# Kernel tuning notes

Hardware: AMD Instinct MI355X
Metric: run time of the kernel (lower is better)

The kernel has to match this reference:

```python
import jax, jax.numpy as jnp
import numpy as np


def setup_inputs() -> dict:
    key = jax.random.key(0)
    ks = jax.random.split(key, 8)
    B, C, W, H = 4, 256, 64, 64
    dqk = C // 8
    s_in = 1.0 / np.sqrt(C)
    return {
        "x": jax.random.normal(ks[0], (B, C, W, H), dtype=jnp.float32),
        "Wq": jax.random.normal(ks[1], (dqk, C), dtype=jnp.float32) * s_in,
        "bq": jnp.zeros((dqk,), dtype=jnp.float32),
        "Wk": jax.random.normal(ks[2], (dqk, C), dtype=jnp.float32) * s_in,
        "bk": jnp.zeros((dqk,), dtype=jnp.float32),
        "Wv": jax.random.normal(ks[3], (C, C), dtype=jnp.float32) * s_in,
        "bv": jnp.zeros((C,), dtype=jnp.float32),
        "gamma": jnp.zeros((1,), dtype=jnp.float32),
    }


def reference(x, Wq, bq, Wk, bk, Wv, bv, gamma):
    B, C, W, H = x.shape
    N = W * H
    xf = x.reshape(B, C, N)  # flatten spatial: B x C x N
    # 1x1 convs == per-pixel linear projections over channels
    q = jnp.einsum("bcn,dc->bnd", xf, Wq) + bq            # B x N x dqk
    k = jnp.einsum("bcn,dc->bdn", xf, Wk) + bk[None, :, None]  # B x dqk x N
    v = jnp.einsum("bcn,dc->bdn", xf, Wv) + bv[None, :, None]  # B x C x N
    # unscaled attention, softmax over keys (last dim)
    attn = jax.nn.softmax(jnp.einsum("bnd,bdm->bnm", q, k), axis=-1)  # B x N x N
    # out[b,c,i] = sum_j v[b,c,j] * attn[b,i,j]  (bmm with attn^T)
    out = jnp.einsum("bcj,bij->bci", v, attn).reshape(B, C, W, H)
    return gamma[0] * out + x
```

## Files before the change

### kernel.cpp

```cpp
#include <hip/hip_runtime.h>

#define BB 4
#define CC 256
#define NN 4096

typedef __attribute__((ext_vector_type(8))) short bh8;
typedef __attribute__((ext_vector_type(4))) float f32x4;

#define WPK_OFF  0
#define BALL_OFF 163840
#define QBF_OFF  165888
#define KBF_OFF  (165888 + 1048576)
#define VBF_OFF  (165888 + 2097152)

typedef const __attribute__((address_space(1))) void* gas_t;
typedef __attribute__((address_space(3))) void* las_t;
__device__ inline void gld16(const void* g, void* l) {
    __builtin_amdgcn_global_load_lds((gas_t)g, (las_t)l, 16, 0, 0);
}

__device__ inline int pack2bf(float a, float b) {
    unsigned ua = __builtin_bit_cast(unsigned, a) + 0x8000u;
    unsigned ub = __builtin_bit_cast(unsigned, b) + 0x8000u;
    return (int)__builtin_amdgcn_perm(ub, ua, 0x07060302u);
}
__device__ inline short f2bf1(float a) {
    return (short)((__builtin_bit_cast(unsigned, a) + 0x8000u) >> 16);
}

__global__ __launch_bounds__(256) void prep_w(const float* __restrict__ Wq,
        const float* __restrict__ bq, const float* __restrict__ Wk,
        const float* __restrict__ bk, const float* __restrict__ Wv,
        const float* __restrict__ bv, short* __restrict__ Wpk,
        float* __restrict__ ball) {
    int tid = blockIdx.x * 256 + threadIdx.x;
    if (tid < 10240) {
        int lane = tid & 63;
        int fc = tid >> 6;
        int mt = fc >> 3, ck = fc & 7;
        int m = mt * 16 + (lane & 15);
        int c0 = ck * 32 + (lane >> 4) * 8;
        const float* wrow;
        if (m < 32)      wrow = Wq + m * 256;
        else if (m < 64) wrow = Wk + (m - 32) * 256;
        else             wrow = Wv + (m - 64) * 256;
        int d[4];
        #pragma unroll
        for (int p = 0; p < 4; ++p)
            d[p] = pack2bf(wrow[c0 + 2 * p], wrow[c0 + 2 * p + 1]);
        *(int4*)(Wpk + tid * 8) = make_int4(d[0], d[1], d[2], d[3]);
    }
    if (tid < 320) {
        float b2 = tid < 32 ? bq[tid] : (tid < 64 ? bk[tid - 32] : bv[tid - 64]);
        ball[tid] = b2;
    }
}

__global__ __launch_bounds__(256) void proj(const float* __restrict__ x,
        const short* __restrict__ Wpk, const float* __restrict__ ball,
        short* __restrict__ qbf, short* __restrict__ kbf,
        short* __restrict__ vbf) {
    int t = threadIdx.x;
    int w = t >> 6, lane = t & 63, quad = lane >> 4, c15 = lane & 15;
    int gw = blockIdx.x * 4 + w;
    int tile = gw >> 1, mh = gw & 1;
    int b = tile >> 8, n0 = (tile & 255) * 16;
    const float* xb = x + (size_t)b * CC * NN;

    bh8 af[8];
    #pragma unroll
    for (int ck = 0; ck < 8; ++ck) {
        float v[8];
        #pragma unroll
        for (int e = 0; e < 8; ++e)
            v[e] = xb[(size_t)(ck * 32 + quad * 8 + e) * NN + n0 + c15];
        int d[4];
        #pragma unroll
        for (int p = 0; p < 4; ++p) d[p] = pack2bf(v[2 * p], v[2 * p + 1]);
        af[ck] = __builtin_bit_cast(bh8, make_int4(d[0], d[1], d[2], d[3]));
    }

    #pragma unroll
    for (int mpi = 0; mpi < 5; ++mpi) {
        int mp = mh * 5 + mpi;
        int mtA = mp * 2, mtB = mp * 2 + 1;
        float blA = ball[mtA * 16 + c15], blB = ball[mtB * 16 + c15];
        f32x4 accA = {blA, blA, blA, blA}, accB = {blB, blB, blB, blB};
        #pragma unroll
        for (int ck = 0; ck < 8; ++ck) {
            bh8 wfA = *(const bh8*)(Wpk + ((mtA * 8 + ck) * 64 + lane) * 8);
            bh8 wfB = *(const bh8*)(Wpk + ((mtB * 8 + ck) * 64 + lane) * 8);
            accA = __builtin_amdgcn_mfma_f32_16x16x32_bf16(af[ck], wfA, accA, 0, 0, 0);
            accB = __builtin_amdgcn_mfma_f32_16x16x32_bf16(af[ck], wfB, accB, 0, 0, 0);
        }
        #pragma unroll
        for (int half = 0; half < 2; ++half) {
            int mt = mp * 2 + half;
            f32x4 acc = half ? accB : accA;
            if (mt < 4) {
                short* dst = (mt < 2) ? qbf : kbf;
                int m = (mt & 1) * 16 + c15;
                #pragma unroll
                for (int r = 0; r < 4; ++r)
                    dst[(size_t)(b * NN + n0 + quad * 4 + r) * 32 + m] = f2bf1(acc[r]);
            } else {
                int c = mt * 16 + c15 - 64;
                int2 pk;
                pk.x = pack2bf(acc[0], acc[1]);
                pk.y = pack2bf(acc[2], acc[3]);
                *(int2*)(vbf + (size_t)b * CC * NN + (size_t)c * NN + n0 + quad * 4) = pk;
            }
        }
    }
}

__global__ __launch_bounds__(512, 2) void flash_attn(
        const short* __restrict__ qbf, const short* __restrict__ kbf,
        const short* __restrict__ vbf, const float* __restrict__ x,
        const float* __restrict__ gamma, float* __restrict__ out) {
    __shared__ char lds[82944];

    int bid = blockIdx.x;
    int b = bid & 3, i0 = (bid >> 2) * 64;
    int t = threadIdx.x;
    int w = t >> 6, lane = t & 63, quad = lane >> 4, c15 = lane & 15;
    int mg = w & 3, nh = w >> 2, jsub = w & 3;

    const short* qb = qbf + (size_t)b * NN * 32;
    const short* kb = kbf + (size_t)b * NN * 32;
    const short* vb = vbf + (size_t)b * CC * NN;

    bh8 qf0 = *(const bh8*)(qb + (size_t)(i0 + nh * 32 + c15) * 32 + quad * 8);
    bh8 qf1 = *(const bh8*)(qb + (size_t)(i0 + nh * 32 + 16 + c15) * 32 + quad * 8);

    int vrow = w * 32 + (lane >> 3);
    int glog = (lane & 7) ^ ((lane >> 3) & 7);
    const short* vsg = vb + (size_t)vrow * NN + glog * 8;
    char* vdst = lds + w * 4096;

    const short* kptr = kb + (size_t)(jsub * 16 + c15) * 32 + quad * 8;

    char* Pt = lds + 65536;
    float* lred = (float*)(lds + 81920);

    f32x4 acc[4][2];
    #pragma unroll
    for (int ms = 0; ms < 4; ++ms) {
        acc[ms][0] = (f32x4){0.f, 0.f, 0.f, 0.f};
        acc[ms][1] = (f32x4){0.f, 0.f, 0.f, 0.f};
    }
    float lsum0 = 0.f, lsum1 = 0.f;
    const f32x4 initc = {-12.f, -12.f, -12.f, -12.f};

    #pragma unroll
    for (int r = 0; r < 4; ++r) gld16(vsg + r * 8 * NN, vdst + r * 1024);
    bh8 kf = *(const bh8*)kptr;
    __syncthreads();

    for (int jt = 0; jt < 64; ++jt) {
        int cur = jt & 1;
        f32x4 sa0 = __builtin_amdgcn_mfma_f32_16x16x32_bf16(kf, qf0, initc, 0, 0, 0);
        f32x4 sa1 = __builtin_amdgcn_mfma_f32_16x16x32_bf16(kf, qf1, initc, 0, 0, 0);
        bh8 kfn = *(const bh8*)(kptr + (size_t)((jt + 1) & 63) * 2048);
        float p0[4], p1[4];
        #pragma unroll
        for (int r = 0; r < 4; ++r) {
            p0[r] = __expf(sa0[r]); lsum0 += p0[r];
            p1[r] = __expf(sa1[r]); lsum1 += p1[r];
        }
        char* Ptc = Pt + cur * 8192;
        int g = jsub * 2 + (quad >> 1);
        int pb0 = (nh * 32 + c15) * 128 + ((g ^ (c15 & 7)) * 16) + (quad & 1) * 8;
        *(int2*)(Ptc + pb0) = make_int2(pack2bf(p0[0], p0[1]), pack2bf(p0[2], p0[3]));
        *(int2*)(Ptc + pb0 + 2048) = make_int2(pack2bf(p1[0], p1[1]), pack2bf(p1[2], p1[3]));

        __syncthreads();

        if (jt < 63) {
            const short* vs = vsg + (jt + 1) * 64;
            char* vd = vdst + ((cur ^ 1) << 15);
            #pragma unroll
            for (int r = 0; r < 4; ++r) gld16(vs + r * 8 * NN, vd + r * 1024);
        }

        const char* Vb = lds + cur * 32768;
        #pragma unroll
        for (int kk = 0; kk < 2; ++kk) {
            int gs = ((kk * 4 + quad) ^ (c15 & 7)) * 16;
            bh8 pfa = *(const bh8*)(Ptc + (nh * 32 + c15) * 128 + gs);
            bh8 pfb = *(const bh8*)(Ptc + (nh * 32 + 16 + c15) * 128 + gs);
            #pragma unroll
            for (int ms = 0; ms < 4; ++ms) {
                int c = mg * 64 + ms * 16 + c15;
                bh8 vf = *(const bh8*)(Vb + c * 128 + gs);
                acc[ms][0] = __builtin_amdgcn_mfma_f32_16x16x32_bf16(vf, pfa, acc[ms][0], 0, 0, 0);
                acc[ms][1] = __builtin_amdgcn_mfma_f32_16x16x32_bf16(vf, pfb, acc[ms][1], 0, 0, 0);
            }
        }
        kf = kfn;
    }

    lsum0 += __shfl_xor(lsum0, 16); lsum0 += __shfl_xor(lsum0, 32);
    lsum1 += __shfl_xor(lsum1, 16); lsum1 += __shfl_xor(lsum1, 32);
    __syncthreads();
    if (lane < 16) {
        lred[w * 32 + lane] = lsum0;
        lred[w * 32 + 16 + lane] = lsum1;
    }
    __syncthreads();
    float l0 = lred[(nh * 4 + 0) * 32 + c15] + lred[(nh * 4 + 1) * 32 + c15]
             + lred[(nh * 4 + 2) * 32 + c15] + lred[(nh * 4 + 3) * 32 + c15];
    float l1 = lred[(nh * 4 + 0) * 32 + 16 + c15] + lred[(nh * 4 + 1) * 32 + 16 + c15]
             + lred[(nh * 4 + 2) * 32 + 16 + c15] + lred[(nh * 4 + 3) * 32 + 16 + c15];
    float linv0 = 1.0f / l0, linv1 = 1.0f / l1;

    float gm = gamma[0];
    const float* xb2 = x + (size_t)b * CC * NN;
    float* ob = out + (size_t)b * CC * NN;
    int ia = i0 + nh * 32 + c15, ib2 = ia + 16;
    #pragma unroll
    for (int ms = 0; ms < 4; ++ms) {
        #pragma unroll
        for (int r = 0; r < 4; ++r) {
            int c = mg * 64 + ms * 16 + quad * 4 + r;
            ob[(size_t)c * NN + ia]  = gm * acc[ms][0][r] * linv0 + xb2[(size_t)c * NN + ia];
            ob[(size_t)c * NN + ib2] = gm * acc[ms][1][r] * linv1 + xb2[(size_t)c * NN + ib2];
        }
    }
}

extern "C" void kernel_launch(void* const* d_in, const int* in_sizes, int n_in,
                              void* d_out, int out_size, void* d_ws, size_t ws_size,
                              hipStream_t stream) {
    const float* x     = (const float*)d_in[0];
    const float* Wq    = (const float*)d_in[1];
    const float* bq    = (const float*)d_in[2];
    const float* Wk    = (const float*)d_in[3];
    const float* bk    = (const float*)d_in[4];
    const float* Wv    = (const float*)d_in[5];
    const float* bv    = (const float*)d_in[6];
    const float* gamma = (const float*)d_in[7];
    float* out = (float*)d_out;
    char*  ws  = (char*)d_ws;
    short* Wpk  = (short*)(ws + WPK_OFF);
    float* ball = (float*)(ws + BALL_OFF);
    short* qbf  = (short*)(ws + QBF_OFF);
    short* kbf  = (short*)(ws + KBF_OFF);
    short* vbf  = (short*)(ws + VBF_OFF);

    prep_w<<<40, 256, 0, stream>>>(Wq, bq, Wk, bk, Wv, bv, Wpk, ball);
    proj<<<512, 256, 0, stream>>>(x, Wpk, ball, qbf, kbf, vbf);
    flash_attn<<<256, 512, 0, stream>>>(qbf, kbf, vbf, x, gamma, out);
}
```

Measured before the change: 142.4 us.

## Restructure attention to 32x32 MFMA with register-held V and LDS-staged proj inputs

```diff
diff --git a/kernel.cpp b/kernel.cpp
--- a/kernel.cpp
+++ b/kernel.cpp
@@ -6,6 +6,7 @@
 
 typedef __attribute__((ext_vector_type(8))) short bh8;
 typedef __attribute__((ext_vector_type(4))) float f32x4;
+typedef __attribute__((ext_vector_type(16))) float f32x16;
 
 #define WPK_OFF  0
 #define BALL_OFF 163840
@@ -60,12 +61,22 @@
         const short* __restrict__ Wpk, const float* __restrict__ ball,
         short* __restrict__ qbf, short* __restrict__ kbf,
         short* __restrict__ vbf) {
+    __shared__ float xs[8192];
     int t = threadIdx.x;
     int w = t >> 6, lane = t & 63, quad = lane >> 4, c15 = lane & 15;
-    int gw = blockIdx.x * 4 + w;
-    int tile = gw >> 1, mh = gw & 1;
-    int b = tile >> 8, n0 = (tile & 255) * 16;
-    const float* xb = x + (size_t)b * CC * NN;
+    int b = blockIdx.x >> 7;
+    int n0 = (blockIdx.x & 127) * 32;
+    const float* xb = x + (size_t)b * CC * NN + n0;
+
+    #pragma unroll
+    for (int r = 0; r < 8; ++r) {
+        const float* src = xb + (size_t)(w * 64 + r * 8 + (lane >> 3)) * NN + (lane & 7) * 4;
+        gld16(src, (char*)xs + w * 8192 + r * 1024);
+    }
+    __syncthreads();
+
+    int ns = w & 1, mh = w >> 1;
+    int nb = ns * 16;
 
     bh8 af[8];
     #pragma unroll
@@ -73,7 +84,7 @@
         float v[8];
         #pragma unroll
         for (int e = 0; e < 8; ++e)
-            v[e] = xb[(size_t)(ck * 32 + quad * 8 + e) * NN + n0 + c15];
+            v[e] = xs[(ck * 32 + quad * 8 + e) * 32 + nb + c15];
         int d[4];
         #pragma unroll
         for (int p = 0; p < 4; ++p) d[p] = pack2bf(v[2 * p], v[2 * p + 1]);
@@ -82,8 +93,7 @@
 
     #pragma unroll
     for (int mpi = 0; mpi < 5; ++mpi) {
-        int mp = mh * 5 + mpi;
-        int mtA = mp * 2, mtB = mp * 2 + 1;
+        int mtA = mh * 10 + mpi * 2, mtB = mtA + 1;
         float blA = ball[mtA * 16 + c15], blB = ball[mtB * 16 + c15];
         f32x4 accA = {blA, blA, blA, blA}, accB = {blB, blB, blB, blB};
         #pragma unroll
@@ -95,136 +105,147 @@
         }
         #pragma unroll
         for (int half = 0; half < 2; ++half) {
-            int mt = mp * 2 + half;
+            int mt = mtA + half;
             f32x4 acc = half ? accB : accA;
             if (mt < 4) {
                 short* dst = (mt < 2) ? qbf : kbf;
                 int m = (mt & 1) * 16 + c15;
                 #pragma unroll
                 for (int r = 0; r < 4; ++r)
-                    dst[(size_t)(b * NN + n0 + quad * 4 + r) * 32 + m] = f2bf1(acc[r]);
+                    dst[(size_t)(b * NN + n0 + nb + quad * 4 + r) * 32 + m] = f2bf1(acc[r]);
             } else {
                 int c = mt * 16 + c15 - 64;
                 int2 pk;
                 pk.x = pack2bf(acc[0], acc[1]);
                 pk.y = pack2bf(acc[2], acc[3]);
-                *(int2*)(vbf + (size_t)b * CC * NN + (size_t)c * NN + n0 + quad * 4) = pk;
-            }
-        }
-    }
-}
-
-__global__ __launch_bounds__(512, 2) void flash_attn(
+                *(int2*)(vbf + (size_t)b * CC * NN + (size_t)c * NN + n0 + nb + quad * 4) = pk;
+            }
+        }
+    }
+}
+
+__global__ __launch_bounds__(256) void flash_attn(
         const short* __restrict__ qbf, const short* __restrict__ kbf,
         const short* __restrict__ vbf, const float* __restrict__ x,
         const float* __restrict__ gamma, float* __restrict__ out) {
-    __shared__ char lds[82944];
+    __shared__ char lds[17408];
 
     int bid = blockIdx.x;
     int b = bid & 3, i0 = (bid >> 2) * 64;
     int t = threadIdx.x;
     int w = t >> 6, lane = t & 63, quad = lane >> 4, c15 = lane & 15;
-    int mg = w & 3, nh = w >> 2, jsub = w & 3;
+    int l31 = lane & 31, l5 = lane >> 5;
 
     const short* qb = qbf + (size_t)b * NN * 32;
     const short* kb = kbf + (size_t)b * NN * 32;
     const short* vb = vbf + (size_t)b * CC * NN;
 
-    bh8 qf0 = *(const bh8*)(qb + (size_t)(i0 + nh * 32 + c15) * 32 + quad * 8);
-    bh8 qf1 = *(const bh8*)(qb + (size_t)(i0 + nh * 32 + 16 + c15) * 32 + quad * 8);
-
-    int vrow = w * 32 + (lane >> 3);
-    int glog = (lane & 7) ^ ((lane >> 3) & 7);
-    const short* vsg = vb + (size_t)vrow * NN + glog * 8;
-    char* vdst = lds + w * 4096;
-
-    const short* kptr = kb + (size_t)(jsub * 16 + c15) * 32 + quad * 8;
-
-    char* Pt = lds + 65536;
-    float* lred = (float*)(lds + 81920);
-
-    f32x4 acc[4][2];
-    #pragma unroll
-    for (int ms = 0; ms < 4; ++ms) {
-        acc[ms][0] = (f32x4){0.f, 0.f, 0.f, 0.f};
-        acc[ms][1] = (f32x4){0.f, 0.f, 0.f, 0.f};
-    }
-    float lsum0 = 0.f, lsum1 = 0.f;
+    bh8 qf[4];
+    #pragma unroll
+    for (int is4 = 0; is4 < 4; ++is4)
+        qf[is4] = *(const bh8*)(qb + (size_t)(i0 + is4 * 16 + c15) * 32 + quad * 8);
+
+    const short* kptr = kb + (size_t)(w * 16 + c15) * 32 + quad * 8;
+
+    const short* vr0 = vb + (size_t)(w * 64 + l31) * NN + l5 * 8;
+    const short* vr1 = vr0 + (size_t)32 * NN;
+
+    f32x16 acc[2][2];
+    #pragma unroll
+    for (int cs = 0; cs < 2; ++cs)
+        #pragma unroll
+        for (int is = 0; is < 2; ++is)
+            #pragma unroll
+            for (int r = 0; r < 16; ++r) acc[cs][is][r] = 0.0f;
+    float lsum[4] = {0.f, 0.f, 0.f, 0.f};
     const f32x4 initc = {-12.f, -12.f, -12.f, -12.f};
 
-    #pragma unroll
-    for (int r = 0; r < 4; ++r) gld16(vsg + r * 8 * NN, vdst + r * 1024);
+    bh8 vA[8], vB[8];
+    #pragma unroll
+    for (int kk = 0; kk < 4; ++kk) {
+        vA[kk]     = *(const bh8*)(vr0 + kk * 16);
+        vA[4 + kk] = *(const bh8*)(vr1 + kk * 16);
+    }
     bh8 kf = *(const bh8*)kptr;
-    __syncthreads();
 
     for (int jt = 0; jt < 64; ++jt) {
-        int cur = jt & 1;
-        f32x4 sa0 = __builtin_amdgcn_mfma_f32_16x16x32_bf16(kf, qf0, initc, 0, 0, 0);
-        f32x4 sa1 = __builtin_amdgcn_mfma_f32_16x16x32_bf16(kf, qf1, initc, 0, 0, 0);
-        bh8 kfn = *(const bh8*)(kptr + (size_t)((jt + 1) & 63) * 2048);
-        float p0[4], p1[4];
-        #pragma unroll
-        for (int r = 0; r < 4; ++r) {
-            p0[r] = __expf(sa0[r]); lsum0 += p0[r];
-            p1[r] = __expf(sa1[r]); lsum1 += p1[r];
-        }
-        char* Ptc = Pt + cur * 8192;
-        int g = jsub * 2 + (quad >> 1);
-        int pb0 = (nh * 32 + c15) * 128 + ((g ^ (c15 & 7)) * 16) + (quad & 1) * 8;
-        *(int2*)(Ptc + pb0) = make_int2(pack2bf(p0[0], p0[1]), pack2bf(p0[2], p0[3]));
-        *(int2*)(Ptc + pb0 + 2048) = make_int2(pack2bf(p1[0], p1[1]), pack2bf(p1[2], p1[3]));
-
+        char* Pc = lds + (jt & 1) * 8192;
+        f32x4 sa[4];
+        #pragma unroll
+        for (int is4 = 0; is4 < 4; ++is4)
+            sa[is4] = __builtin_amdgcn_mfma_f32_16x16x32_bf16(kf, qf[is4], initc, 0, 0, 0);
+        kf = *(const bh8*)(kptr + (size_t)((jt + 1) & 63) * 2048);
+        int jg = w * 2 + (quad >> 1);
+        #pragma unroll
+        for (int is4 = 0; is4 < 4; ++is4) {
+            float p[4];
+            #pragma unroll
+            for (int r = 0; r < 4; ++r) { p[r] = __expf(sa[is4][r]); lsum[is4] += p[r]; }
+            int i_ = is4 * 16 + c15;
+            *(int2*)(Pc + i_ * 128 + ((jg ^ (c15 & 7)) * 16) + (quad & 1) * 8) =
+                make_int2(pack2bf(p[0], p[1]), pack2bf(p[2], p[3]));
+        }
         __syncthreads();
 
         if (jt < 63) {
-            const short* vs = vsg + (jt + 1) * 64;
-            char* vd = vdst + ((cur ^ 1) << 15);
-            #pragma unroll
-            for (int r = 0; r < 4; ++r) gld16(vs + r * 8 * NN, vd + r * 1024);
-        }
-
-        const char* Vb = lds + cur * 32768;
-        #pragma unroll
-        for (int kk = 0; kk < 2; ++kk) {
-            int gs = ((kk * 4 + quad) ^ (c15 & 7)) * 16;
-            bh8 pfa = *(const bh8*)(Ptc + (nh * 32 + c15) * 128 + gs);
-            bh8 pfb = *(const bh8*)(Ptc + (nh * 32 + 16 + c15) * 128 + gs);
-            #pragma unroll
-            for (int ms = 0; ms < 4; ++ms) {
-                int c = mg * 64 + ms * 16 + c15;
-                bh8 vf = *(const bh8*)(Vb + c * 128 + gs);
-                acc[ms][0] = __builtin_amdgcn_mfma_f32_16x16x32_bf16(vf, pfa, acc[ms][0], 0, 0, 0);
-                acc[ms][1] = __builtin_amdgcn_mfma_f32_16x16x32_bf16(vf, pfb, acc[ms][1], 0, 0, 0);
-            }
-        }
-        kf = kfn;
-    }
-
-    lsum0 += __shfl_xor(lsum0, 16); lsum0 += __shfl_xor(lsum0, 32);
-    lsum1 += __shfl_xor(lsum1, 16); lsum1 += __shfl_xor(lsum1, 32);
+            const short* v0n = vr0 + (size_t)(jt + 1) * 64;
+            const short* v1n = vr1 + (size_t)(jt + 1) * 64;
+            #pragma unroll
+            for (int kk = 0; kk < 4; ++kk) {
+                vB[kk]     = *(const bh8*)(v0n + kk * 16);
+                vB[4 + kk] = *(const bh8*)(v1n + kk * 16);
+            }
+        }
+
+        bh8 pf[2][4];
+        #pragma unroll
+        for (int is = 0; is < 2; ++is)
+            #pragma unroll
+            for (int kk = 0; kk < 4; ++kk) {
+                int irow = is * 32 + l31;
+                int slot = (kk * 2 + l5) ^ (irow & 7);
+                pf[is][kk] = *(const bh8*)(Pc + irow * 128 + slot * 16);
+            }
+        #pragma unroll
+        for (int kk = 0; kk < 4; ++kk) {
+            acc[0][0] = __builtin_amdgcn_mfma_f32_32x32x16_bf16(vA[kk],     pf[0][kk], acc[0][0], 0, 0, 0);
+            acc[0][1] = __builtin_amdgcn_mfma_f32_32x32x16_bf16(vA[kk],     pf[1][kk], acc[0][1], 0, 0, 0);
+            acc[1][0] = __builtin_amdgcn_mfma_f32_32x32x16_bf16(vA[4 + kk], pf[0][kk], acc[1][0], 0, 0, 0);
+            acc[1][1] = __builtin_amdgcn_mfma_f32_32x32x16_bf16(vA[4 + kk], pf[1][kk], acc[1][1], 0, 0, 0);
+        }
+        #pragma unroll
+        for (int q2 = 0; q2 < 8; ++q2) vA[q2] = vB[q2];
+    }
+
+    #pragma unroll
+    for (int is4 = 0; is4 < 4; ++is4) {
+        lsum[is4] += __shfl_xor(lsum[is4], 16);
+        lsum[is4] += __shfl_xor(lsum[is4], 32);
+    }
+    float* lred = (float*)(lds + 16384);
     __syncthreads();
     if (lane < 16) {
-        lred[w * 32 + lane] = lsum0;
-        lred[w * 32 + 16 + lane] = lsum1;
+        #pragma unroll
+        for (int is4 = 0; is4 < 4; ++is4) lred[w * 64 + is4 * 16 + lane] = lsum[is4];
     }
     __syncthreads();
-    float l0 = lred[(nh * 4 + 0) * 32 + c15] + lred[(nh * 4 + 1) * 32 + c15]
-             + lred[(nh * 4 + 2) * 32 + c15] + lred[(nh * 4 + 3) * 32 + c15];
-    float l1 = lred[(nh * 4 + 0) * 32 + 16 + c15] + lred[(nh * 4 + 1) * 32 + 16 + c15]
-             + lred[(nh * 4 + 2) * 32 + 16 + c15] + lred[(nh * 4 + 3) * 32 + 16 + c15];
-    float linv0 = 1.0f / l0, linv1 = 1.0f / l1;
 
     float gm = gamma[0];
     const float* xb2 = x + (size_t)b * CC * NN;
     float* ob = out + (size_t)b * CC * NN;
-    int ia = i0 + nh * 32 + c15, ib2 = ia + 16;
-    #pragma unroll
-    for (int ms = 0; ms < 4; ++ms) {
-        #pragma unroll
-        for (int r = 0; r < 4; ++r) {
-            int c = mg * 64 + ms * 16 + quad * 4 + r;
-            ob[(size_t)c * NN + ia]  = gm * acc[ms][0][r] * linv0 + xb2[(size_t)c * NN + ia];
-            ob[(size_t)c * NN + ib2] = gm * acc[ms][1][r] * linv1 + xb2[(size_t)c * NN + ib2];
+    #pragma unroll
+    for (int is = 0; is < 2; ++is) {
+        int i_l = is * 32 + l31;
+        float lt = lred[i_l] + lred[64 + i_l] + lred[128 + i_l] + lred[192 + i_l];
+        float linv = 1.0f / lt;
+        int i = i0 + i_l;
+        #pragma unroll
+        for (int cs = 0; cs < 2; ++cs) {
+            #pragma unroll
+            for (int r = 0; r < 16; ++r) {
+                int c = w * 64 + cs * 32 + (r & 3) + 8 * (r >> 2) + 4 * l5;
+                ob[(size_t)c * NN + i] = gm * acc[cs][is][r] * linv + xb2[(size_t)c * NN + i];
+            }
         }
     }
 }
@@ -250,5 +271,5 @@
 
     prep_w<<<40, 256, 0, stream>>>(Wq, bq, Wk, bk, Wv, bv, Wpk, ball);
     proj<<<512, 256, 0, stream>>>(x, Wpk, ball, qbf, kbf, vbf);
-    flash_attn<<<256, 512, 0, stream>>>(qbf, kbf, vbf, x, gamma, out);
-}
+    flash_attn<<<256, 256, 0, stream>>>(qbf, kbf, vbf, x, gamma, out);
+}
```

New measurement: 202.7 us. +42.3%, slower.
